# Performance work log

Measured on AMD Instinct MI355X. Metric: run time of the kernel, lower is better.

## Reference

```python
import jax, jax.numpy as jnp
import numpy as np

# Model dims
N = 4096      # tokens (batch 2 * seq 2048, flattened)
D = 1024      # d_model
E = 16        # num_expert
K = 2         # top_k
H = 2048      # expert hidden dim
CAP = 1024


def setup_inputs() -> dict:
    key = jax.random.key(0)
    k0, k1, k2, k3 = jax.random.split(key, 4)
    s_d = 1.0 / np.sqrt(D).astype(np.float32)
    s_h = 1.0 / np.sqrt(H).astype(np.float32)
    return {
        "moe_inp": jax.random.normal(k0, (N, D), jnp.float32),
        "Wg": jax.random.normal(k1, (D, E), jnp.float32) * s_d,   # NaiveGate linear
        "bg": jnp.zeros((E,), jnp.float32),
        "W1": jax.random.normal(k2, (E, D, H), jnp.float32) * s_d,  # per-expert FFN layer 1
        "b1": jnp.zeros((E, H), jnp.float32),
        "W2": jax.random.normal(k3, (E, H, D), jnp.float32) * s_h,  # per-expert FFN layer 2
        "b2": jnp.zeros((E, D), jnp.float32),
    }


def reference(moe_inp, Wg, bg, W1, b1, W2, b2):
    # ---- gate (NaiveGate): linear -> top_k -> softmax over selected logits ----
    logits = moe_inp @ Wg + bg                      # [N, E]
    top_v, top_i = jax.lax.top_k(logits, K)         # [N, K]
    gate_score = jax.nn.softmax(top_v, axis=-1)     # [N, K]

    # ---- dispatch (MOEScatter): sort tokens into contiguous per-expert buffers ----
    flat_e = top_i.reshape(-1)                      # [N*K] expert id per assignment
    oh = jax.nn.one_hot(flat_e, E, dtype=jnp.int32)               # [N*K, E]
    pos_all = jnp.cumsum(oh, axis=0) - oh                          # rank within expert
    pos = jnp.take_along_axis(pos_all, flat_e[:, None], axis=1)[:, 0]  # [N*K]
    valid = pos < CAP
    pos_safe = jnp.where(valid, pos, CAP)           # out-of-range -> dropped by scatter

    x_rep = jnp.repeat(moe_inp, K, axis=0)          # [N*K, D]
    x_e = jnp.zeros((E, CAP, D), moe_inp.dtype).at[flat_e, pos_safe].set(
        x_rep, mode='drop')                          # [E, CAP, D]

    # ---- per-expert grouped FFN (expert_fn) ----
    h = jax.nn.gelu(jnp.einsum('ecd,edh->ech', x_e, W1) + b1[:, None, :])  # [E, CAP, H]
    y_e = jnp.einsum('ech,ehd->ecd', h, W2) + b2[:, None, :]               # [E, CAP, D]

    # ---- gather (MOEGather) + weighted combine by gate scores ----
    y_tok = y_e.at[flat_e, pos_safe].get(mode='fill', fill_value=0.0)      # [N*K, D]
    y_tok = y_tok * valid[:, None].astype(y_tok.dtype)
    y = y_tok.reshape(N, K, D)
    return jnp.einsum('nkd,nk->nd', y, gate_score)  # [N, D]
```

## Files before the change

### kernel.cpp

```cpp
#include <hip/hip_runtime.h>

#define N_TOK 4096
#define DMODEL 1024
#define NEXP 16
#define HDIM 2048
#define CAP 1024

typedef __attribute__((ext_vector_type(8))) short frag8;
typedef __attribute__((ext_vector_type(4))) float f32x4;
typedef __attribute__((ext_vector_type(8))) unsigned short us8;

__device__ __forceinline__ unsigned short f2bf(float x) {
  unsigned u = __builtin_bit_cast(unsigned, x);
  u += 0x7fffu + ((u >> 16) & 1u);
  return (unsigned short)(u >> 16);
}
__device__ __forceinline__ float bf2f(unsigned short b) {
  unsigned u = ((unsigned)b) << 16;
  return __builtin_bit_cast(float, u);
}
__device__ __forceinline__ void load_lds16(const void* g, void* l) {
  __builtin_amdgcn_global_load_lds((const __attribute__((address_space(1))) void*)g,
                                   (__attribute__((address_space(3))) void*)l, 16, 0, 0);
}
#define SBAR0 __builtin_amdgcn_sched_barrier(0)

__global__ __launch_bounds__(256) void gate_logits_kernel(
    const float* __restrict__ x, const float* __restrict__ Wg, const float* __restrict__ bg,
    int* __restrict__ a_e, float* __restrict__ a_gate)
{
  int wid = threadIdx.x >> 6, l = threadIdx.x & 63;
  int n = blockIdx.x * 4 + wid;
  const float* xr = x + (size_t)n * DMODEL;
  float acc[NEXP];
#pragma unroll
  for (int e = 0; e < NEXP; ++e) acc[e] = 0.f;
#pragma unroll
  for (int q = 0; q < 4; ++q) {
    float4 xv = *(const float4*)(xr + q * 256 + l * 4);
    const float* wr = Wg + (size_t)(q * 256 + l * 4) * NEXP;
#pragma unroll
    for (int j = 0; j < 4; ++j) {
      float xs = j == 0 ? xv.x : j == 1 ? xv.y : j == 2 ? xv.z : xv.w;
      const float4* w4 = (const float4*)(wr + j * NEXP);
#pragma unroll
      for (int qq = 0; qq < 4; ++qq) {
        float4 w = w4[qq];
        acc[qq*4+0] += xs * w.x; acc[qq*4+1] += xs * w.y;
        acc[qq*4+2] += xs * w.z; acc[qq*4+3] += xs * w.w;
      }
    }
  }
#pragma unroll
  for (int e = 0; e < NEXP; ++e) {
    float v = acc[e];
#pragma unroll
    for (int off = 32; off > 0; off >>= 1) v += __shfl_xor(v, off, 64);
    acc[e] = v + bg[e];
  }
  if (l == 0) {
    int i1 = 0; float v1 = acc[0];
#pragma unroll
    for (int e = 1; e < NEXP; ++e) if (acc[e] > v1) { v1 = acc[e]; i1 = e; }
    int i2 = -1; float v2 = -1e30f;
#pragma unroll
    for (int e = 0; e < NEXP; ++e) if (e != i1 && acc[e] > v2) { v2 = acc[e]; i2 = e; }
    float e2 = __expf(v2 - v1);
    float inv = 1.f / (1.f + e2);
    a_e[n*2] = i1;   a_gate[n*2] = inv;
    a_e[n*2+1] = i2; a_gate[n*2+1] = e2 * inv;
  }
}

__global__ __launch_bounds__(256) void assign_kernel(
    const int* __restrict__ a_e, int* __restrict__ a_slot,
    int* __restrict__ tok_of_slot, int* __restrict__ cnt)
{
  __shared__ int c;
  if (threadIdx.x == 0) c = 0;
  __syncthreads();
  int eid = blockIdx.x;
  for (int j = threadIdx.x; j < N_TOK * 2; j += 256) {
    if (a_e[j] == eid) {
      int p = atomicAdd(&c, 1);
      a_slot[j] = p;
      if (p < CAP) tok_of_slot[eid * CAP + p] = j >> 1;
    }
  }
  __syncthreads();
  if (threadIdx.x == 0) cnt[eid] = c;
}

__global__ __launch_bounds__(256) void gather_kernel(
    const float* __restrict__ x, const int* __restrict__ cnt,
    const int* __restrict__ tok_of_slot, unsigned short* __restrict__ Xe)
{
  int rid = blockIdx.x * 2 + (threadIdx.x >> 7);
  int tl = threadIdx.x & 127;
  int e = rid >> 10, slot = rid & (CAP - 1);
  int c = cnt[e]; if (c > CAP) c = CAP;
  if (slot >= c) return;
  int tok = tok_of_slot[rid];
  const float4* xs = (const float4*)(x + (size_t)tok * DMODEL + tl * 8);
  float4 u = xs[0], v = xs[1];
  us8 p;
  p[0]=f2bf(u.x); p[1]=f2bf(u.y); p[2]=f2bf(u.z); p[3]=f2bf(u.w);
  p[4]=f2bf(v.x); p[5]=f2bf(v.y); p[6]=f2bf(v.z); p[7]=f2bf(v.w);
  int kt = tl >> 3, s = tl & 7;
  int row = slot & 127, rt = slot >> 7;
  size_t off = ((size_t)((e*8 + rt)*16 + kt)) * 8192 + (size_t)row*64 + ((s ^ (row & 7)) << 3);
  *(us8*)&Xe[off] = p;
}

template<int KT, int NT, bool GELU, bool OUT_BLOCKED>
__global__ __launch_bounds__(256, 3) void gemm_kernel(
    const unsigned short* __restrict__ Aimg, const float* __restrict__ W,
    unsigned short* __restrict__ OutU, const float* __restrict__ bias,
    const int* __restrict__ cnt)
{
  constexpr int LDW = NT * 128;
  __shared__ __align__(16) char smem[32768];
  constexpr int NBLK = NEXP * 8 * NT;
  int bid = blockIdx.x;
  int item = (bid & 7) * (NBLK / 8) + (bid >> 3);
  int e = item / (8 * NT), rem = item % (8 * NT);
  int mt = rem / NT, nt = rem % NT;
  int mcnt = cnt[e]; if (mcnt > CAP) mcnt = CAP;
  if (mt * 128 >= mcnt) return;
  int t = threadIdx.x, l = t & 63, wid = t >> 6;
  int wm = wid >> 1, wn = wid & 1;
  int rA = l & 15, g = l >> 4, r7 = rA & 7;
  int sw0 = (g ^ r7) << 4, sw1 = ((g + 4) ^ r7) << 4;

  const char* asrc = (const char*)(Aimg + (size_t)(e * 8 + mt) * KT * 8192);
  int brow = t & 127;
  int bk0 = (t >> 7) * 32;
  int bs0 = bk0 >> 3;
  int bsig = brow & 7;
  const float* wsrc = W + (size_t)e * (KT * 64) * LDW + (size_t)nt * 128 + brow;
  float br[32];

  auto loadB = [&](int kt) {
    const float* p = wsrc + (size_t)(kt * 64 + bk0) * LDW;
#pragma unroll
    for (int j = 0; j < 32; ++j) br[j] = p[(size_t)j * LDW];
  };
  auto writeB = [&]() {
    char* lB = smem + 16384;
#pragma unroll
    for (int c2 = 0; c2 < 4; ++c2) {
      us8 p8;
#pragma unroll
      for (int j = 0; j < 8; ++j) p8[j] = f2bf(br[c2 * 8 + j]);
      *(us8*)(lB + brow * 128 + (((bs0 + c2) ^ bsig) << 4)) = p8;
    }
  };
  auto stageA = [&](int kt) {
    const char* s = asrc + (size_t)kt * 16384;
    load_lds16(s + t * 16,         smem + t * 16);
    load_lds16(s + 4096 + t * 16,  smem + 4096 + t * 16);
    load_lds16(s + 8192 + t * 16,  smem + 8192 + t * 16);
    load_lds16(s + 12288 + t * 16, smem + 12288 + t * 16);
  };

  f32x4 acc[4][4] = {};
  const char* bA = smem + (wm * 64 + rA) * 128;
  const char* bB = smem + 16384 + (wn * 64 + rA) * 128;

  auto compute = [&]() {
    frag8 bfr[4][2];
#pragma unroll
    for (int n16 = 0; n16 < 4; ++n16) {
      bfr[n16][0] = *(const frag8*)(bB + n16 * 2048 + sw0);
      bfr[n16][1] = *(const frag8*)(bB + n16 * 2048 + sw1);
    }
    __builtin_amdgcn_s_setprio(1);
#pragma unroll
    for (int m16 = 0; m16 < 4; ++m16) {
      frag8 a0 = *(const frag8*)(bA + m16 * 2048 + sw0);
      frag8 a1 = *(const frag8*)(bA + m16 * 2048 + sw1);
#pragma unroll
      for (int n16 = 0; n16 < 4; ++n16) {
        acc[m16][n16] = __builtin_amdgcn_mfma_f32_16x16x32_bf16(a0, bfr[n16][0], acc[m16][n16], 0, 0, 0);
        acc[m16][n16] = __builtin_amdgcn_mfma_f32_16x16x32_bf16(a1, bfr[n16][1], acc[m16][n16], 0, 0, 0);
      }
    }
    __builtin_amdgcn_s_setprio(0);
  };

  loadB(0); SBAR0;
  stageA(0); SBAR0;
  asm volatile("s_waitcnt vmcnt(4)" ::: "memory");
  writeB();
  loadB(1); SBAR0;
  asm volatile("s_waitcnt vmcnt(32)" ::: "memory");
  asm volatile("s_waitcnt lgkmcnt(0)" ::: "memory");
  SBAR0; __builtin_amdgcn_s_barrier(); SBAR0;

  for (int kt = 0; kt < KT; ++kt) {
    compute();
    if (kt + 1 < KT) {
      SBAR0; __builtin_amdgcn_s_barrier(); SBAR0;
      stageA(kt + 1); SBAR0;
      asm volatile("s_waitcnt vmcnt(4)" ::: "memory");
      writeB();
      int kL = (kt + 2 < KT) ? kt + 2 : KT - 1;
      loadB(kL); SBAR0;
      asm volatile("s_waitcnt vmcnt(32)" ::: "memory");
      asm volatile("s_waitcnt lgkmcnt(0)" ::: "memory");
      SBAR0; __builtin_amdgcn_s_barrier(); SBAR0;
    }
  }
  SBAR0; __builtin_amdgcn_s_barrier(); SBAR0;

  float bv[4];
#pragma unroll
  for (int n16 = 0; n16 < 4; ++n16)
    bv[n16] = bias[e * LDW + nt * 128 + wn * 64 + n16 * 16 + rA];

  char* wb = smem + wid * 8192;
  if constexpr (OUT_BLOCKED) {
#pragma unroll
    for (int m16 = 0; m16 < 4; ++m16)
#pragma unroll
      for (int n16 = 0; n16 < 4; ++n16)
#pragma unroll
        for (int rr = 0; rr < 4; ++rr) {
          float xv = acc[m16][n16][rr] + bv[n16];
          if (GELU) {
            float u = 0.7978845608028654f * (xv + 0.044715f * xv * xv * xv);
            xv = xv / (1.f + __expf(-2.f * u));
          }
          int row = m16 * 16 + g * 4 + rr;
          int col = n16 * 16 + rA;
          *(unsigned short*)(wb + row * 128 + (((col >> 3) ^ (row & 7)) << 4) + (col & 7) * 2) = f2bf(xv);
        }
    asm volatile("s_waitcnt lgkmcnt(0)" ::: "memory");
    size_t ob = ((size_t)(e * 8 + mt) * (2 * NT) + nt * 2 + wn) * 8192;
#pragma unroll
    for (int it = 0; it < 8; ++it) {
      int row = it * 8 + (l >> 3), p = l & 7;
      us8 v = *(const us8*)(wb + row * 128 + p * 16);
      *(us8*)&OutU[ob + (size_t)(wm * 64 + row) * 64 + p * 8] = v;
    }
  } else {
#pragma unroll
    for (int m16 = 0; m16 < 4; ++m16)
#pragma unroll
      for (int n16 = 0; n16 < 4; ++n16)
#pragma unroll
        for (int rr = 0; rr < 4; ++rr) {
          int row = m16 * 16 + g * 4 + rr;
          int col = n16 * 16 + rA;
          *(unsigned short*)(wb + row * 128 + col * 2) = f2bf(acc[m16][n16][rr] + bv[n16]);
        }
    asm volatile("s_waitcnt lgkmcnt(0)" ::: "memory");
#pragma unroll
    for (int it = 0; it < 8; ++it) {
      int row = it * 8 + (l >> 3), p = l & 7;
      us8 v = *(const us8*)(wb + row * 128 + p * 16);
      *(us8*)&OutU[(size_t)(e * CAP + mt * 128 + wm * 64 + row) * LDW
                   + nt * 128 + wn * 64 + p * 8] = v;
    }
  }
}

__global__ __launch_bounds__(256) void combine_kernel(
    const unsigned short* __restrict__ ye, const int* __restrict__ a_e,
    const int* __restrict__ a_slot, const float* __restrict__ a_gate, float* __restrict__ out)
{
  int n = blockIdx.x, t = threadIdx.x;
  int e0 = a_e[n*2], e1 = a_e[n*2+1];
  int s0 = a_slot[n*2], s1 = a_slot[n*2+1];
  float g0 = a_gate[n*2], g1 = a_gate[n*2+1];
  float r[4] = {0.f, 0.f, 0.f, 0.f};
  if (s0 < CAP) {
    ushort4 v = *(const ushort4*)&ye[(size_t)(e0*CAP + s0)*DMODEL + t*4];
    r[0] += g0*bf2f(v.x); r[1] += g0*bf2f(v.y); r[2] += g0*bf2f(v.z); r[3] += g0*bf2f(v.w);
  }
  if (s1 < CAP) {
    ushort4 v = *(const ushort4*)&ye[(size_t)(e1*CAP + s1)*DMODEL + t*4];
    r[0] += g1*bf2f(v.x); r[1] += g1*bf2f(v.y); r[2] += g1*bf2f(v.z); r[3] += g1*bf2f(v.w);
  }
  float4 o; o.x = r[0]; o.y = r[1]; o.z = r[2]; o.w = r[3];
  *(float4*)&out[(size_t)n*DMODEL + t*4] = o;
}

extern "C" void kernel_launch(void* const* d_in, const int* in_sizes, int n_in,
                              void* d_out, int out_size, void* d_ws, size_t ws_size,
                              hipStream_t stream) {
  const float* x  = (const float*)d_in[0];
  const float* Wg = (const float*)d_in[1];
  const float* bg = (const float*)d_in[2];
  const float* W1 = (const float*)d_in[3];
  const float* b1 = (const float*)d_in[4];
  const float* W2 = (const float*)d_in[5];
  const float* b2 = (const float*)d_in[6];
  float* out = (float*)d_out;
  char* ws = (char*)d_ws;

  unsigned short* Xe = (unsigned short*)(ws);
  unsigned short* hB = (unsigned short*)(ws + 33554432);
  unsigned short* ye = (unsigned short*)(ws + 100663296);
  int* cnt           = (int*)(ws + 134217728);
  int* tok           = (int*)(ws + 134217792);
  int* a_e           = (int*)(ws + 134283328);
  int* a_slot        = (int*)(ws + 134316096);
  float* a_gate      = (float*)(ws + 134348864);

  gate_logits_kernel<<<1024, 256, 0, stream>>>(x, Wg, bg, a_e, a_gate);
  assign_kernel<<<16, 256, 0, stream>>>(a_e, a_slot, tok, cnt);
  gather_kernel<<<8192, 256, 0, stream>>>(x, cnt, tok, Xe);
  gemm_kernel<16, 16, true,  true ><<<2048, 256, 0, stream>>>(Xe, W1, hB, b1, cnt);
  gemm_kernel<32, 8,  false, false><<<1024, 256, 0, stream>>>(hB, W2, ye, b2, cnt);
  combine_kernel<<<4096, 256, 0, stream>>>(ye, a_e, a_slot, a_gate, out);
}
```

Before: 234.8 us.

## Double-buffer the A tile in LDS to prefetch two k-steps ahead

Adds a second 16KB LDS buffer for the activation (A) tile so the global-to-LDS copy for step k+2 is issued while step k+1's buffer is already resident. The waitcnt and barrier schedule is reworked so that the A load latency overlaps compute rather than being waited on right after each barrier. LDS use grows from 32KB to 48KB per block, which may reduce how many blocks fit on a CU given launch_bounds(256,3).

```diff
diff --git a/kernel.cpp b/kernel.cpp
--- a/kernel.cpp
+++ b/kernel.cpp
@@ -119,7 +119,7 @@
     const int* __restrict__ cnt)
 {
   constexpr int LDW = NT * 128;
-  __shared__ __align__(16) char smem[32768];
+  __shared__ __align__(16) char smem[49152];
   constexpr int NBLK = NEXP * 8 * NT;
   int bid = blockIdx.x;
   int item = (bid & 7) * (NBLK / 8) + (bid >> 3);
@@ -146,7 +146,7 @@
     for (int j = 0; j < 32; ++j) br[j] = p[(size_t)j * LDW];
   };
   auto writeB = [&]() {
-    char* lB = smem + 16384;
+    char* lB = smem + 32768;
 #pragma unroll
     for (int c2 = 0; c2 < 4; ++c2) {
       us8 p8;
@@ -155,19 +155,21 @@
       *(us8*)(lB + brow * 128 + (((bs0 + c2) ^ bsig) << 4)) = p8;
     }
   };
-  auto stageA = [&](int kt) {
+  auto stageA = [&](char* dst, int kt) {
     const char* s = asrc + (size_t)kt * 16384;
-    load_lds16(s + t * 16,         smem + t * 16);
-    load_lds16(s + 4096 + t * 16,  smem + 4096 + t * 16);
-    load_lds16(s + 8192 + t * 16,  smem + 8192 + t * 16);
-    load_lds16(s + 12288 + t * 16, smem + 12288 + t * 16);
+    load_lds16(s + t * 16,         dst + t * 16);
+    load_lds16(s + 4096 + t * 16,  dst + 4096 + t * 16);
+    load_lds16(s + 8192 + t * 16,  dst + 8192 + t * 16);
+    load_lds16(s + 12288 + t * 16, dst + 12288 + t * 16);
   };
 
   f32x4 acc[4][4] = {};
-  const char* bA = smem + (wm * 64 + rA) * 128;
-  const char* bB = smem + 16384 + (wn * 64 + rA) * 128;
-
-  auto compute = [&]() {
+  char* A0 = smem;
+  char* A1 = smem + 16384;
+
+  auto compute = [&](const char* aBuf) {
+    const char* bA = aBuf + (wm * 64 + rA) * 128;
+    const char* bB = smem + 32768 + (wn * 64 + rA) * 128;
     frag8 bfr[4][2];
 #pragma unroll
     for (int n16 = 0; n16 < 4; ++n16) {
@@ -189,28 +191,33 @@
   };
 
   loadB(0); SBAR0;
-  stageA(0); SBAR0;
+  stageA(A0, 0); SBAR0;
   asm volatile("s_waitcnt vmcnt(4)" ::: "memory");
   writeB();
   loadB(1); SBAR0;
-  asm volatile("s_waitcnt vmcnt(32)" ::: "memory");
+  stageA(A1, 1); SBAR0;
+  asm volatile("s_waitcnt vmcnt(36)" ::: "memory");
   asm volatile("s_waitcnt lgkmcnt(0)" ::: "memory");
   SBAR0; __builtin_amdgcn_s_barrier(); SBAR0;
 
+  int cur = 0;
   for (int kt = 0; kt < KT; ++kt) {
-    compute();
+    compute(cur ? A1 : A0);
     if (kt + 1 < KT) {
+      asm volatile("s_waitcnt vmcnt(4)" ::: "memory");
       SBAR0; __builtin_amdgcn_s_barrier(); SBAR0;
-      stageA(kt + 1); SBAR0;
-      asm volatile("s_waitcnt vmcnt(4)" ::: "memory");
       writeB();
-      int kL = (kt + 2 < KT) ? kt + 2 : KT - 1;
-      loadB(kL); SBAR0;
-      asm volatile("s_waitcnt vmcnt(32)" ::: "memory");
+      int k2 = (kt + 2 < KT) ? kt + 2 : KT - 1;
+      loadB(k2); SBAR0;
+      stageA(cur ? A1 : A0, k2); SBAR0;
+      asm volatile("s_waitcnt vmcnt(36)" ::: "memory");
       asm volatile("s_waitcnt lgkmcnt(0)" ::: "memory");
       SBAR0; __builtin_amdgcn_s_barrier(); SBAR0;
-    }
-  }
+      cur ^= 1;
+    }
+  }
+  asm volatile("s_waitcnt vmcnt(0)" ::: "memory");
+  asm volatile("s_waitcnt lgkmcnt(0)" ::: "memory");
   SBAR0; __builtin_amdgcn_s_barrier(); SBAR0;
 
   float bv[4];
```

Result: faster. 227.8 us (-3.0%).
